# Optimization experiments

Hardware: AMD Instinct MI355X
Metric: run time of the kernel (lower is better)

## Reference

```python
import jax, jax.numpy as jnp
import numpy as np

NUM_HEADS = 12
DROP_RATIO = 0.25
LN_EPS = 1e-5


def _layernorm(x, g, b):
    m = jnp.mean(x, axis=-1, keepdims=True)
    v = jnp.var(x, axis=-1, keepdims=True)
    return (x - m) * jax.lax.rsqrt(v + LN_EPS) * g + b


def setup_inputs() -> dict:
    key = jax.random.key(0)
    ks = jax.random.split(key, 12)
    B, N, C = 16, 785, 768
    H = 4 * C
    s = 0.02
    return {
        "x": jax.random.normal(ks[0], (B, N, C), dtype=jnp.float32),
        "ln1_g": jnp.ones((C,), jnp.float32),
        "ln1_b": jnp.zeros((C,), jnp.float32),
        "w_qkv": jax.random.normal(ks[1], (C, 3 * C), jnp.float32) * s,  # qkv_bias=False
        "w_proj": jax.random.normal(ks[2], (C, C), jnp.float32) * s,
        "b_proj": jnp.zeros((C,), jnp.float32),
        "ln2_g": jnp.ones((C,), jnp.float32),
        "ln2_b": jnp.zeros((C,), jnp.float32),
        "w_fc1": jax.random.normal(ks[3], (C, H), jnp.float32) * s,
        "b_fc1": jnp.zeros((H,), jnp.float32),
        "w_fc2": jax.random.normal(ks[4], (H, C), jnp.float32) * s,
        "b_fc2": jnp.zeros((C,), jnp.float32),
    }


def _block(x, ln1_g, ln1_b, w_qkv, w_proj, b_proj, ln2_g, ln2_b,
           w_fc1, b_fc1, w_fc2, b_fc2):
    B, N, C = x.shape
    Hh = NUM_HEADS
    Dh = C // Hh
    scale = Dh ** -0.5
    target = N - int(N * DROP_RATIO)  # kept KV length (incl. CLS)

    h = _layernorm(x, ln1_g, ln1_b)
    qkv = (h @ w_qkv).reshape(B, N, 3, Hh, Dh).transpose(2, 0, 3, 1, 4)
    q, k, v = qkv[0], qkv[1], qkv[2]  # each [B, H, N, Dh]

    # 'low' branch: L2-norm token scoring on non-CLS k tokens, keep top (target-1)
    rem_k = k[:, :, 1:, :]
    rem_v = v[:, :, 1:, :]
    scores = jnp.linalg.norm(rem_k, axis=-1) / Dh  # [B, H, N-1]
    _, idx = jax.lax.top_k(scores, target - 1)
    idx = jnp.sort(idx, axis=-1)  # restore original token order
    idx_e = idx[..., None]
    new_k = jnp.concatenate(
        [k[:, :, :1, :], jnp.take_along_axis(rem_k, idx_e, axis=2)], axis=2)
    new_v = jnp.concatenate(
        [v[:, :, :1, :], jnp.take_along_axis(rem_v, idx_e, axis=2)], axis=2)

    attn = jnp.einsum('bhnd,bhmd->bhnm', q, new_k) * scale
    attn = jax.nn.softmax(attn, axis=-1)
    o = jnp.einsum('bhnm,bhmd->bhnd', attn, new_v)
    o = o.transpose(0, 2, 1, 3).reshape(B, N, C)
    o = o @ w_proj + b_proj
    x = x + o  # drop_path = 0

    h2 = _layernorm(x, ln2_g, ln2_b)
    m = jax.nn.gelu(h2 @ w_fc1 + b_fc1, approximate=False) @ w_fc2 + b_fc2
    return x + m


def reference(x, ln1_g, ln1_b, w_qkv, w_proj, b_proj, ln2_g, ln2_b,
              w_fc1, b_fc1, w_fc2, b_fc2):
    return _block(x, ln1_g, ln1_b, w_qkv, w_proj, b_proj, ln2_g, ln2_b,
                  w_fc1, b_fc1, w_fc2, b_fc2)
```

## Files before the change

kernel.cpp:

```cpp
#include <hip/hip_runtime.h>

#define B_ 16
#define NTOK 785
#define C_ 768
#define HH 12
#define DH 64
#define BHN (B_*HH)
#define KVLEN 589
#define KVPAD 640
#define MROWS (B_*785)
#define HID 3072

typedef __bf16  bf16x8  __attribute__((ext_vector_type(8)));
typedef short   short4v __attribute__((ext_vector_type(4)));
typedef float   f32x4   __attribute__((ext_vector_type(4)));
typedef int     int4v   __attribute__((ext_vector_type(4)));
typedef unsigned short u16;
typedef signed char i8;

__device__ __forceinline__ u16 f2b(float f) {
  unsigned u = __builtin_bit_cast(unsigned, f);
  u = u + 0x7FFFu + ((u >> 16) & 1u);
  return (u16)(u >> 16);
}

#define SH_I8   (127.0f / 6.0f)
#define SW1_I8  (127.0f / 0.125f)
#define DEQ1    ((6.0f * 0.125f) / (127.0f * 127.0f))
#define SG_I8   (127.0f / 4.0f)
#define SW2_I8  (127.0f / 0.12f)
#define DEQ2    ((4.0f * 0.12f) / (127.0f * 127.0f))

#define QSCALE  0.18033688011112042f

__device__ __forceinline__ i8 f2i8(float v, float s) {
  float q = rintf(v * s);
  q = fminf(127.0f, fmaxf(-127.0f, q));
  return (i8)(int)q;
}

__device__ __forceinline__ float gelu_f(float x) {
  float ax = fabsf(x) * 0.70710678118654752f;
  float t  = __builtin_amdgcn_rcpf(1.0f + 0.3275911f * ax);
  float y  = t * (0.254829592f + t * (-0.284496736f + t * (1.421413741f +
             t * (-1.453152027f + t * 1.061405429f))));
  float er = 1.0f - y * __expf(-ax * ax);
  er = copysignf(er, x);
  return 0.5f * x * (1.0f + er);
}

#define AS1C(p) ((const __attribute__((address_space(1))) void*)(p))
#define AS3(p)  ((__attribute__((address_space(3))) void*)(p))
#define SWZ(row, g) ((row)*64 + ((((g) ^ ((row)&7))) << 3))
#define SWZ8B(row, g) ((row)*128 + ((((g) ^ ((row)&7))) << 4))

#define OFF_H   ((size_t)0)
#define OFF_KF  ((size_t)19292160)
#define OFF_QB  (OFF_KF + (size_t)38584320)
#define OFF_VB  (OFF_QB + (size_t)19292160)
#define OFF_KP  (OFF_VB + (size_t)19292160)
#define OFF_VP  (OFF_KP + (size_t)15728640)
#define OFF_OB  (OFF_VP + (size_t)15728640)
#define OFF_WQ  (OFF_OB + (size_t)19292160)
#define OFF_WP  (OFF_WQ + (size_t)3538944)
#define OFF_W1  (OFF_WP + (size_t)1179648)
#define OFF_W2  (OFF_W1 + (size_t)4718592)
#define OFF_SC  (OFF_W2 + (size_t)4718592)
#define OFF_IX  (OFF_SC + (size_t)602112)
#define OFF_G   OFF_KF

__global__ __launch_bounds__(256)
void transpose_cast(const float* __restrict__ w, u16* __restrict__ wt, int K, int N) {
  __shared__ float T[64][65];
  const int k0 = blockIdx.x * 64, n0 = blockIdx.y * 64;
  const int tid = threadIdx.x;
  const int cc = tid & 63, rr = tid >> 6;
#pragma unroll
  for (int i = 0; i < 16; ++i) {
    int r = rr + i * 4;
    T[r][cc] = w[(size_t)(k0 + r) * N + n0 + cc];
  }
  __syncthreads();
#pragma unroll
  for (int i = 0; i < 16; ++i) {
    int r = rr + i * 4;
    wt[(size_t)(n0 + r) * K + k0 + cc] = f2b(T[cc][r]);
  }
}

__global__ __launch_bounds__(256)
void transpose_quant(const float* __restrict__ w, i8* __restrict__ wt, int K, int N,
                     float scale) {
  __shared__ float T[64][65];
  const int k0 = blockIdx.x * 64, n0 = blockIdx.y * 64;
  const int tid = threadIdx.x;
  const int cc = tid & 63, rr = tid >> 6;
#pragma unroll
  for (int i = 0; i < 16; ++i) {
    int r = rr + i * 4;
    T[r][cc] = w[(size_t)(k0 + r) * N + n0 + cc];
  }
  __syncthreads();
#pragma unroll
  for (int i = 0; i < 16; ++i) {
    int r = rr + i * 4;
    wt[(size_t)(n0 + r) * K + k0 + cc] = f2i8(T[cc][r], scale);
  }
}

__global__ __launch_bounds__(256)
void ln_kernel(const float* __restrict__ x, const float* __restrict__ g,
               const float* __restrict__ b, u16* __restrict__ out) {
  const int row = blockIdx.x;
  const int tid = threadIdx.x;
  const float* xr = x + (size_t)row * C_;
  float v0 = xr[tid], v1 = xr[tid + 256], v2 = xr[tid + 512];
  float sum = v0 + v1 + v2;
  float sq  = v0 * v0 + v1 * v1 + v2 * v2;
#pragma unroll
  for (int o = 32; o > 0; o >>= 1) { sum += __shfl_xor(sum, o); sq += __shfl_xor(sq, o); }
  __shared__ float rs[4], rq[4];
  int w = tid >> 6;
  if ((tid & 63) == 0) { rs[w] = sum; rq[w] = sq; }
  __syncthreads();
  sum = rs[0] + rs[1] + rs[2] + rs[3];
  sq  = rq[0] + rq[1] + rq[2] + rq[3];
  float mean = sum * (1.0f / C_);
  float var  = sq * (1.0f / C_) - mean * mean;
  float rstd = rsqrtf(var + 1e-5f);
  u16* orow = out + (size_t)row * C_;
  orow[tid]       = f2b((v0 - mean) * rstd * g[tid]       + b[tid]);
  orow[tid + 256] = f2b((v1 - mean) * rstd * g[tid + 256] + b[tid + 256]);
  orow[tid + 512] = f2b((v2 - mean) * rstd * g[tid + 512] + b[tid + 512]);
}

__global__ __launch_bounds__(256)
void ln_kernel_i8(const float* __restrict__ x, const float* __restrict__ g,
                  const float* __restrict__ b, i8* __restrict__ out) {
  const int row = blockIdx.x;
  const int tid = threadIdx.x;
  const float* xr = x + (size_t)row * C_;
  float v0 = xr[tid], v1 = xr[tid + 256], v2 = xr[tid + 512];
  float sum = v0 + v1 + v2;
  float sq  = v0 * v0 + v1 * v1 + v2 * v2;
#pragma unroll
  for (int o = 32; o > 0; o >>= 1) { sum += __shfl_xor(sum, o); sq += __shfl_xor(sq, o); }
  __shared__ float rs[4], rq[4];
  int w = tid >> 6;
  if ((tid & 63) == 0) { rs[w] = sum; rq[w] = sq; }
  __syncthreads();
  sum = rs[0] + rs[1] + rs[2] + rs[3];
  sq  = rq[0] + rq[1] + rq[2] + rq[3];
  float mean = sum * (1.0f / C_);
  float var  = sq * (1.0f / C_) - mean * mean;
  float rstd = rsqrtf(var + 1e-5f);
  i8* orow = out + (size_t)row * C_;
  orow[tid]       = f2i8((v0 - mean) * rstd * g[tid]       + b[tid],       SH_I8);
  orow[tid + 256] = f2i8((v1 - mean) * rstd * g[tid + 256] + b[tid + 256], SH_I8);
  orow[tid + 512] = f2i8((v2 - mean) * rstd * g[tid + 512] + b[tid + 512], SH_I8);
}

template<int EPI>
__global__ __launch_bounds__(256, 2)
void gemm128(const u16* __restrict__ A, const u16* __restrict__ Bt,
             int M, int N, int K,
             const float* __restrict__ bias, const float* __restrict__ addsrc,
             float* __restrict__ outf, u16* __restrict__ outb,
             u16* __restrict__ qb, u16* __restrict__ kb, u16* __restrict__ vb,
             float* __restrict__ sc) {
  __shared__ u16 As[128 * 64];
  __shared__ u16 Bs[128 * 64];
  const int tid = threadIdx.x;
  const int lane = tid & 63;
  const int w = tid >> 6;
  const int wm = w >> 1, wn = w & 1;
  const int l15 = lane & 15;
  const int hi = lane >> 4;

  const int CN = (N + 127) >> 7;
  const int nwg = gridDim.x * gridDim.y;
  const int orig = blockIdx.x + blockIdx.y * gridDim.x;
  const int q = nwg >> 3, r8 = nwg & 7;
  const int xcd = orig & 7, pos = orig >> 3;
  const int wgid = (xcd < r8 ? xcd * (q + 1) : r8 * (q + 1) + (xcd - r8) * q) + pos;
  const int m0 = (wgid / CN) * 128;
  const int n0 = (wgid - (wgid / CN) * CN) * 128;

  const int srow = tid >> 3;
  const int sseg = tid & 7;

  f32x4 acc[4][4] = {};

  for (int kt = 0; kt < K; kt += 64) {
    __syncthreads();
#pragma unroll
    for (int i = 0; i < 4; ++i) {
      int row = i * 32 + srow;
      int gseg = sseg ^ (row & 7);
      int gr = m0 + row; if (gr >= M) gr = M - 1;
      int flat = i * 256 + tid;
      __builtin_amdgcn_global_load_lds(AS1C(A  + (size_t)gr * K         + kt + gseg * 8),
                                       AS3(&As[flat * 8]), 16, 0, 0);
      __builtin_amdgcn_global_load_lds(AS1C(Bt + (size_t)(n0 + row) * K + kt + gseg * 8),
                                       AS3(&Bs[flat * 8]), 16, 0, 0);
    }
    __syncthreads();
#pragma unroll
    for (int kk = 0; kk < 2; ++kk) {
      bf16x8 a[4], b[4];
#pragma unroll
      for (int mi = 0; mi < 4; ++mi)
        a[mi] = *reinterpret_cast<const bf16x8*>(&As[SWZ(wm * 64 + mi * 16 + l15, kk * 4 + hi)]);
#pragma unroll
      for (int ni = 0; ni < 4; ++ni)
        b[ni] = *reinterpret_cast<const bf16x8*>(&Bs[SWZ(wn * 64 + ni * 16 + l15, kk * 4 + hi)]);
#pragma unroll
      for (int mi = 0; mi < 4; ++mi)
#pragma unroll
        for (int ni = 0; ni < 4; ++ni)
          acc[mi][ni] = __builtin_amdgcn_mfma_f32_16x16x32_bf16(a[mi], b[ni], acc[mi][ni], 0, 0, 0);
    }
  }

#pragma unroll
  for (int mi = 0; mi < 4; ++mi) {
#pragma unroll
    for (int ni = 0; ni < 4; ++ni) {
#pragma unroll
      for (int j = 0; j < 4; ++j) {
        int r = m0 + wm * 64 + mi * 16 + hi * 4 + j;
        int c = n0 + wn * 64 + ni * 16 + l15;
        if (r < M) {
          float v = acc[mi][ni][j];
          if (EPI == 0) {
            int sec = (c >= 1536) ? 2 : (c >= 768 ? 1 : 0);
            int cm = c - sec * 768;
            int hh = cm >> 6, d = cm & 63;
            int bb = r / NTOK; int nn = r - bb * NTOK;
            size_t addr = (((size_t)(bb * HH + hh)) * NTOK + nn) * DH + d;
            if (sec == 0)      qb[addr] = f2b(v * QSCALE);
            else if (sec == 1) kb[addr] = f2b(v);
            else               vb[addr] = f2b(v);
          } else {
            size_t o = (size_t)r * N + c;
            outf[o] = v + bias[c] + addsrc[o];
          }
        }
      }
    }
  }

  if (EPI == 0) {
    int csec = n0 + wn * 64;
    if (csec >= 768 && csec < 1536) {
      int hh = (csec - 768) >> 6;
#pragma unroll
      for (int mi = 0; mi < 4; ++mi) {
#pragma unroll
        for (int j = 0; j < 4; ++j) {
          float ss = 0.0f;
#pragma unroll
          for (int ni = 0; ni < 4; ++ni) { float v = acc[mi][ni][j]; ss += v * v; }
          ss += __shfl_xor(ss, 1); ss += __shfl_xor(ss, 2);
          ss += __shfl_xor(ss, 4); ss += __shfl_xor(ss, 8);
          int r = m0 + wm * 64 + mi * 16 + hi * 4 + j;
          if (l15 == 0 && r < M) {
            int bb = r / NTOK, nn = r - bb * NTOK;
            if (nn >= 1)
              sc[(size_t)(bb * HH + hh) * 784 + nn - 1] = sqrtf(ss) * (1.0f / 64.0f);
          }
        }
      }
    }
  }
}

template<int EPI>
__global__ __launch_bounds__(256, 2)
void gemm128_i8(const i8* __restrict__ A, const i8* __restrict__ Bt,
                int M, int N, int K, float deq,
                const float* __restrict__ bias, const float* __restrict__ addsrc,
                float* __restrict__ outf, i8* __restrict__ outq) {
  __shared__ i8 As[128 * 128];
  __shared__ i8 Bs[128 * 128];
  const int tid = threadIdx.x;
  const int lane = tid & 63;
  const int w = tid >> 6;
  const int wm = w >> 1, wn = w & 1;
  const int l15 = lane & 15;
  const int hi = lane >> 4;

  const int CN = (N + 127) >> 7;
  const int nwg = gridDim.x * gridDim.y;
  const int orig = blockIdx.x + blockIdx.y * gridDim.x;
  const int q = nwg >> 3, r8 = nwg & 7;
  const int xcd = orig & 7, pos = orig >> 3;
  const int wgid = (xcd < r8 ? xcd * (q + 1) : r8 * (q + 1) + (xcd - r8) * q) + pos;
  const int m0 = (wgid / CN) * 128;
  const int n0 = (wgid - (wgid / CN) * CN) * 128;

  const int srow = tid >> 3;
  const int sg   = tid & 7;

  int4v acc[4][4] = {};

  for (int kt = 0; kt < K; kt += 128) {
    __syncthreads();
#pragma unroll
    for (int i = 0; i < 4; ++i) {
      int row = i * 32 + srow;
      int gsw = sg ^ (row & 7);
      int gr = m0 + row; if (gr >= M) gr = M - 1;
      int flat = i * 256 + tid;
      __builtin_amdgcn_global_load_lds(AS1C(A  + (size_t)gr * K         + kt + gsw * 16),
                                       AS3(&As[flat * 16]), 16, 0, 0);
      __builtin_amdgcn_global_load_lds(AS1C(Bt + (size_t)(n0 + row) * K + kt + gsw * 16),
                                       AS3(&Bs[flat * 16]), 16, 0, 0);
    }
    __syncthreads();
#pragma unroll
    for (int kk = 0; kk < 2; ++kk) {
      int4v a[4], b[4];
#pragma unroll
      for (int mi = 0; mi < 4; ++mi) {
        int R = wm * 64 + mi * 16 + l15;
        a[mi] = *reinterpret_cast<const int4v*>(&As[SWZ8B(R, kk * 4 + hi)]);
      }
#pragma unroll
      for (int ni = 0; ni < 4; ++ni) {
        int R = wn * 64 + ni * 16 + l15;
        b[ni] = *reinterpret_cast<const int4v*>(&Bs[SWZ8B(R, kk * 4 + hi)]);
      }
#pragma unroll
      for (int mi = 0; mi < 4; ++mi)
#pragma unroll
        for (int ni = 0; ni < 4; ++ni)
          acc[mi][ni] = __builtin_amdgcn_mfma_i32_16x16x64_i8(a[mi], b[ni], acc[mi][ni], 0, 0, 0);
    }
  }

#pragma unroll
  for (int mi = 0; mi < 4; ++mi) {
#pragma unroll
    for (int ni = 0; ni < 4; ++ni) {
#pragma unroll
      for (int j = 0; j < 4; ++j) {
        int r = m0 + wm * 64 + mi * 16 + hi * 4 + j;
        int c = n0 + wn * 64 + ni * 16 + l15;
        if (r < M) {
          float t = (float)acc[mi][ni][j] * deq + bias[c];
          if (EPI == 2) {
            outq[(size_t)r * N + c] = f2i8(gelu_f(t), SG_I8);
          } else {
            size_t o = (size_t)r * N + c;
            outf[o] = t + addsrc[o];
          }
        }
      }
    }
  }
}

__global__ __launch_bounds__(512)
void topk_kernel(const float* __restrict__ scores, int* __restrict__ idxb) {
  const int bh = blockIdx.x;
  const int tid = threadIdx.x;
  __shared__ float ss[1024];
  __shared__ int   sid[1024];
  __shared__ int   sid2[1024];
  for (int i = tid; i < 1024; i += 512) {
    ss[i]  = (i < 784) ? scores[bh * 784 + i] : -__builtin_inff();
    sid[i] = i;
  }
  for (int k = 2; k <= 1024; k <<= 1) {
    for (int j = k >> 1; j > 0; j >>= 1) {
      __syncthreads();
      for (int i = tid; i < 1024; i += 512) {
        int ixj = i ^ j;
        if (ixj > i) {
          float s1 = ss[i], s2 = ss[ixj];
          int   i1 = sid[i], i2 = sid[ixj];
          bool keep = (s1 > s2) || (s1 == s2 && i1 < i2);
          bool doSwap = ((i & k) == 0) ? !keep : keep;
          if (doSwap) { ss[i] = s2; ss[ixj] = s1; sid[i] = i2; sid[ixj] = i1; }
        }
      }
    }
  }
  __syncthreads();
  for (int i = tid; i < 1024; i += 512)
    sid2[i] = (i < 588) ? sid[i] : 0x7FFFFFFF;
  for (int k = 2; k <= 1024; k <<= 1) {
    for (int j = k >> 1; j > 0; j >>= 1) {
      __syncthreads();
      for (int i = tid; i < 1024; i += 512) {
        int ixj = i ^ j;
        if (ixj > i) {
          int a = sid2[i], b2 = sid2[ixj];
          bool keep = (a < b2);
          bool doSwap = ((i & k) == 0) ? !keep : keep;
          if (doSwap) { sid2[i] = b2; sid2[ixj] = a; }
        }
      }
    }
  }
  __syncthreads();
  for (int i = tid; i < 588; i += 512) idxb[bh * 588 + i] = sid2[i];
}

__global__ __launch_bounds__(256)
void gather_kernel(const u16* __restrict__ kb, const u16* __restrict__ vb,
                   const int* __restrict__ idxb, u16* __restrict__ kp, u16* __restrict__ vpT) {
  __shared__ u16 T[64 * 64];
  const int bh = blockIdx.x, chunk = blockIdx.y, t = threadIdx.x;
  {
    int jl = t >> 2, d0 = (t & 3) * 16;
    int j = chunk * 64 + jl;
    int n = (j == 0) ? 0 : (j <= 588 ? idxb[bh * 588 + j - 1] + 1 : -1);
    int4v k0 = {}, k1 = {}, v0 = {}, v1 = {};
    if (n >= 0) {
      size_t src = ((size_t)bh * NTOK + n) * DH + d0;
      k0 = *reinterpret_cast<const int4v*>(&kb[src]);
      k1 = *reinterpret_cast<const int4v*>(&kb[src + 8]);
      v0 = *reinterpret_cast<const int4v*>(&vb[src]);
      v1 = *reinterpret_cast<const int4v*>(&vb[src + 8]);
    }
    size_t kdst = ((size_t)bh * KVPAD + j) * DH + d0;
    *reinterpret_cast<int4v*>(&kp[kdst])     = k0;
    *reinterpret_cast<int4v*>(&kp[kdst + 8]) = k1;
    *reinterpret_cast<int4v*>(&T[jl * 64 + d0])     = v0;
    *reinterpret_cast<int4v*>(&T[jl * 64 + d0 + 8]) = v1;
  }
  __syncthreads();
  {
    int d = t & 63, kvo = (t >> 6) * 16;
    const int swp = ((d >> 3) & 1) * 4;
    alignas(16) u16 tmp[16];
#pragma unroll
    for (int i = 0; i < 16; ++i) tmp[i ^ swp] = T[(kvo + i) * 64 + d];
    size_t dst = ((size_t)bh * 64 + d) * KVPAD + chunk * 64 + kvo;
    *reinterpret_cast<int4v*>(&vpT[dst])     = *reinterpret_cast<int4v*>(&tmp[0]);
    *reinterpret_cast<int4v*>(&vpT[dst + 8]) = *reinterpret_cast<int4v*>(&tmp[8]);
  }
}

__global__ __launch_bounds__(256)
void attn_kernel(const u16* __restrict__ qb, const u16* __restrict__ kp,
                 const u16* __restrict__ vpT, u16* __restrict__ ob) {
  __shared__ u16 Qs[64 * 64];
  __shared__ u16 Ks[64 * 64];
  __shared__ u16 VTs[64 * 64];
  const int tid = threadIdx.x;
  const int lane = tid & 63;
  const int w = tid >> 6;
  const int l15 = lane & 15;
  const int hi = lane >> 4;
  const int hswp = (l15 >> 3) & 1;

  const int nwg = gridDim.x;
  const int orig = blockIdx.x;
  const int q = nwg >> 3, r8 = nwg & 7;
  const int xcd = orig & 7, pos = orig >> 3;
  const int wgid = (xcd < r8 ? xcd * (q + 1) : r8 * (q + 1) + (xcd - r8) * q) + pos;
  const int bh = wgid / 13;
  const int n0 = (wgid - bh * 13) * 64;

#pragma unroll
  for (int i = 0; i < 2; ++i) {
    int flat = i * 256 + tid;
    int row = flat >> 3, g = flat & 7;
    int4v val = {};
    if (n0 + row < NTOK)
      val = *reinterpret_cast<const int4v*>(qb + ((size_t)bh * NTOK + n0 + row) * DH + g * 8);
    *reinterpret_cast<int4v*>(&Qs[SWZ(row, g)]) = val;
  }
  __syncthreads();
  bf16x8 q0 = *reinterpret_cast<const bf16x8*>(&Qs[SWZ(w * 16 + l15, hi)]);
  bf16x8 q1 = *reinterpret_cast<const bf16x8*>(&Qs[SWZ(w * 16 + l15, 4 + hi)]);

  float m_run = -__builtin_inff(), l_run = 0.0f;
  f32x4 oa[4] = {};

#define ATTN_STEP(KVT, MASKED)                                                    \
  {                                                                               \
    int4v kr[2], vr[2];                                                           \
    _Pragma("unroll")                                                             \
    for (int i = 0; i < 2; ++i) {                                                 \
      int flat = i * 256 + tid;                                                   \
      int row = flat >> 3, g = flat & 7;                                          \
      kr[i] = *reinterpret_cast<const int4v*>(                                    \
          kp  + ((size_t)bh * KVPAD + (KVT) * 64 + row) * DH + g * 8);            \
      vr[i] = *reinterpret_cast<const int4v*>(                                    \
          vpT + ((size_t)bh * 64 + row) * KVPAD + (KVT) * 64 + g * 8);            \
    }                                                                             \
    __syncthreads();                                                              \
    _Pragma("unroll")                                                             \
    for (int i = 0; i < 2; ++i) {                                                 \
      int flat = i * 256 + tid;                                                   \
      int row = flat >> 3, g = flat & 7;                                          \
      *reinterpret_cast<int4v*>(&Ks[SWZ(row, g)])  = kr[i];                       \
      *reinterpret_cast<int4v*>(&VTs[SWZ(row, g)]) = vr[i];                       \
    }                                                                             \
    __syncthreads();                                                              \
    f32x4 st[4];                                                                  \
    _Pragma("unroll")                                                             \
    for (int ft = 0; ft < 4; ++ft) {                                              \
      bf16x8 a0 = *reinterpret_cast<const bf16x8*>(&Ks[SWZ(ft * 16 + l15, hi)]);  \
      bf16x8 a1 = *reinterpret_cast<const bf16x8*>(&Ks[SWZ(ft * 16 + l15, 4 + hi)]); \
      f32x4 cfr = {};                                                             \
      cfr = __builtin_amdgcn_mfma_f32_16x16x32_bf16(a0, q0, cfr, 0, 0, 0);        \
      cfr = __builtin_amdgcn_mfma_f32_16x16x32_bf16(a1, q1, cfr, 0, 0, 0);        \
      if (MASKED) {                                                               \
        _Pragma("unroll")                                                         \
        for (int j = 0; j < 4; ++j) {                                             \
          int kv = (KVT) * 64 + ft * 16 + hi * 4 + j;                             \
          if (kv >= KVLEN) cfr[j] = -3.0e38f;                                     \
        }                                                                         \
      }                                                                           \
      st[ft] = cfr;                                                               \
    }                                                                             \
    float mx = fmaxf(fmaxf(st[0][0], st[0][1]), fmaxf(st[0][2], st[0][3]));       \
    _Pragma("unroll")                                                             \
    for (int ft = 1; ft < 4; ++ft)                                                \
      mx = fmaxf(mx, fmaxf(fmaxf(st[ft][0], st[ft][1]), fmaxf(st[ft][2], st[ft][3]))); \
    mx = fmaxf(mx, __shfl_xor(mx, 16));                                           \
    mx = fmaxf(mx, __shfl_xor(mx, 32));                                           \
    float m_new = fmaxf(m_run, mx);                                               \
    float alpha = exp2f(m_run - m_new);                                           \
    float psum = 0.0f;                                                            \
    short4v pb[4];                                                                \
    _Pragma("unroll")                                                             \
    for (int ft = 0; ft < 4; ++ft) {                                              \
      _Pragma("unroll")                                                           \
      for (int j = 0; j < 4; ++j) {                                               \
        float p = exp2f(st[ft][j] - m_new);                                       \
        psum += p;                                                                \
        pb[ft][j] = (short)(u16)(__builtin_bit_cast(unsigned, p) >> 16);          \
      }                                                                           \
    }                                                                             \
    psum += __shfl_xor(psum, 16);                                                 \
    psum += __shfl_xor(psum, 32);                                                 \
    l_run = l_run * alpha + psum;                                                 \
    m_run = m_new;                                                                \
    _Pragma("unroll")                                                             \
    for (int df = 0; df < 4; ++df) {                                              \
      oa[df][0] *= alpha; oa[df][1] *= alpha; oa[df][2] *= alpha; oa[df][3] *= alpha; \
    }                                                                             \
    _Pragma("unroll")                                                             \
    for (int df = 0; df < 4; ++df) {                                              \
      _Pragma("unroll")                                                           \
      for (int ft = 0; ft < 4; ++ft) {                                            \
        short4v va = *reinterpret_cast<const short4v*>(                           \
            &VTs[SWZ(df * 16 + l15, ft * 2 + (hi >> 1)) + (((hi & 1) ^ hswp)) * 4]); \
        oa[df] = __builtin_amdgcn_mfma_f32_16x16x16bf16_1k(va, pb[ft], oa[df], 0, 0, 0); \
      }                                                                           \
    }                                                                             \
  }

  for (int kvt = 0; kvt < 9; ++kvt) {
    ATTN_STEP(kvt, false)
  }
  ATTN_STEP(9, true)
#undef ATTN_STEP

  int n = n0 + w * 16 + l15;
  if (n < NTOK) {
    float inv = 1.0f / l_run;
    int bb = bh / HH, hh = bh - bb * HH;
    size_t base = ((size_t)bb * NTOK + n) * C_ + hh * DH;
#pragma unroll
    for (int df = 0; df < 4; ++df) {
      short4v pv;
#pragma unroll
      for (int j = 0; j < 4; ++j) pv[j] = (short)f2b(oa[df][j] * inv);
      *reinterpret_cast<short4v*>(ob + base + df * 16 + hi * 4) = pv;
    }
  }
}

extern "C" void kernel_launch(void* const* d_in, const int* in_sizes, int n_in,
                              void* d_out, int out_size, void* d_ws, size_t ws_size,
                              hipStream_t stream) {
  const float* x     = (const float*)d_in[0];
  const float* ln1g  = (const float*)d_in[1];
  const float* ln1b  = (const float*)d_in[2];
  const float* wqkv  = (const float*)d_in[3];
  const float* wproj = (const float*)d_in[4];
  const float* bproj = (const float*)d_in[5];
  const float* ln2g  = (const float*)d_in[6];
  const float* ln2b  = (const float*)d_in[7];
  const float* wfc1  = (const float*)d_in[8];
  const float* bfc1  = (const float*)d_in[9];
  const float* wfc2  = (const float*)d_in[10];
  const float* bfc2  = (const float*)d_in[11];
  float* out = (float*)d_out;
  char* wsb = (char*)d_ws;

  u16*   h     = (u16*)(wsb + OFF_H);
  i8*    hq    = (i8*)(wsb + OFF_H);
  u16*   kb    = (u16*)(wsb + OFF_KF);
  u16*   qb    = (u16*)(wsb + OFF_QB);
  u16*   vb    = (u16*)(wsb + OFF_VB);
  u16*   kp    = (u16*)(wsb + OFF_KP);
  u16*   vpT   = (u16*)(wsb + OFF_VP);
  u16*   ob    = (u16*)(wsb + OFF_OB);
  u16*   wqT   = (u16*)(wsb + OFF_WQ);
  u16*   wpT   = (u16*)(wsb + OFF_WP);
  i8*    w1q   = (i8*)(wsb + OFF_W1);
  i8*    w2q   = (i8*)(wsb + OFF_W2);
  float* sc    = (float*)(wsb + OFF_SC);
  int*   idxb  = (int*)(wsb + OFF_IX);
  i8*    gq    = (i8*)(wsb + OFF_G);

  transpose_cast<<<dim3(768 / 64, 2304 / 64), 256, 0, stream>>>(wqkv, wqT, 768, 2304);
  transpose_cast<<<dim3(768 / 64, 768 / 64),  256, 0, stream>>>(wproj, wpT, 768, 768);
  transpose_quant<<<dim3(768 / 64, 3072 / 64), 256, 0, stream>>>(wfc1, w1q, 768, 3072, SW1_I8);
  transpose_quant<<<dim3(3072 / 64, 768 / 64), 256, 0, stream>>>(wfc2, w2q, 3072, 768, SW2_I8);

  ln_kernel<<<MROWS, 256, 0, stream>>>(x, ln1g, ln1b, h);

  gemm128<0><<<dim3(2304 / 128, 99), 256, 0, stream>>>(h, wqT, MROWS, 2304, 768,
      nullptr, nullptr, nullptr, nullptr, qb, kb, vb, sc);

  topk_kernel<<<BHN, 512, 0, stream>>>(sc, idxb);
  gather_kernel<<<dim3(BHN, KVPAD / 64), 256, 0, stream>>>(kb, vb, idxb, kp, vpT);

  attn_kernel<<<BHN * 13, 256, 0, stream>>>(qb, kp, vpT, ob);

  gemm128<1><<<dim3(768 / 128, 99), 256, 0, stream>>>(ob, wpT, MROWS, 768, 768,
      bproj, x, out, nullptr, nullptr, nullptr, nullptr, nullptr);

  ln_kernel_i8<<<MROWS, 256, 0, stream>>>(out, ln2g, ln2b, hq);

  gemm128_i8<2><<<dim3(3072 / 128, 99), 256, 0, stream>>>(hq, w1q, MROWS, 3072, 768,
      DEQ1, bfc1, nullptr, nullptr, gq);

  gemm128_i8<3><<<dim3(768 / 128, 99), 256, 0, stream>>>(gq, w2q, MROWS, 768, 3072,
      DEQ2, bfc2, out, out, nullptr);
}
```

Measured before the change: 391.3 us.

## Process 128 query rows per attention workgroup to reuse K/V tiles

Each attention workgroup now handles 128 query rows instead of 64, with every wave computing two 16-row query blocks against the same K and V tiles held in shared memory. This halves the number of K/V tile loads from global memory and the barriers per query row, and gives each wave more independent MFMA work to interleave. In exchange it raises register pressure, since two sets of accumulators and softmax state are live, and cuts the grid from 13 to 7 chunks per head, which wastes more padded rows in the last chunk and lowers workgroup count.

```diff
diff --git a/kernel.cpp b/kernel.cpp
--- a/kernel.cpp
+++ b/kernel.cpp
@@ -10,6 +10,7 @@
 #define KVPAD 640
 #define MROWS (B_*785)
 #define HID 3072
+#define QCH 7
 
 typedef __bf16  bf16x8  __attribute__((ext_vector_type(8)));
 typedef short   short4v __attribute__((ext_vector_type(4)));
@@ -447,7 +448,7 @@
 __global__ __launch_bounds__(256)
 void attn_kernel(const u16* __restrict__ qb, const u16* __restrict__ kp,
                  const u16* __restrict__ vpT, u16* __restrict__ ob) {
-  __shared__ u16 Qs[64 * 64];
+  __shared__ u16 Qs[128 * 64];
   __shared__ u16 Ks[64 * 64];
   __shared__ u16 VTs[64 * 64];
   const int tid = threadIdx.x;
@@ -462,11 +463,11 @@
   const int q = nwg >> 3, r8 = nwg & 7;
   const int xcd = orig & 7, pos = orig >> 3;
   const int wgid = (xcd < r8 ? xcd * (q + 1) : r8 * (q + 1) + (xcd - r8) * q) + pos;
-  const int bh = wgid / 13;
-  const int n0 = (wgid - bh * 13) * 64;
-
-#pragma unroll
-  for (int i = 0; i < 2; ++i) {
+  const int bh = wgid / QCH;
+  const int n0 = (wgid - bh * QCH) * 128;
+
+#pragma unroll
+  for (int i = 0; i < 4; ++i) {
     int flat = i * 256 + tid;
     int row = flat >> 3, g = flat & 7;
     int4v val = {};
@@ -475,11 +476,15 @@
     *reinterpret_cast<int4v*>(&Qs[SWZ(row, g)]) = val;
   }
   __syncthreads();
-  bf16x8 q0 = *reinterpret_cast<const bf16x8*>(&Qs[SWZ(w * 16 + l15, hi)]);
-  bf16x8 q1 = *reinterpret_cast<const bf16x8*>(&Qs[SWZ(w * 16 + l15, 4 + hi)]);
-
-  float m_run = -__builtin_inff(), l_run = 0.0f;
-  f32x4 oa[4] = {};
+  const int rA = w * 32 + l15, rB = rA + 16;
+  bf16x8 qa0 = *reinterpret_cast<const bf16x8*>(&Qs[SWZ(rA, hi)]);
+  bf16x8 qa1 = *reinterpret_cast<const bf16x8*>(&Qs[SWZ(rA, 4 + hi)]);
+  bf16x8 qb0 = *reinterpret_cast<const bf16x8*>(&Qs[SWZ(rB, hi)]);
+  bf16x8 qb1 = *reinterpret_cast<const bf16x8*>(&Qs[SWZ(rB, 4 + hi)]);
+
+  float mA = -__builtin_inff(), lA = 0.0f;
+  float mB = -__builtin_inff(), lB = 0.0f;
+  f32x4 oaA[4] = {}, oaB[4] = {};
 
 #define ATTN_STEP(KVT, MASKED)                                                    \
   {                                                                               \
@@ -502,49 +507,57 @@
       *reinterpret_cast<int4v*>(&VTs[SWZ(row, g)]) = vr[i];                       \
     }                                                                             \
     __syncthreads();                                                              \
-    f32x4 st[4];                                                                  \
+    f32x4 stA[4], stB[4];                                                         \
     _Pragma("unroll")                                                             \
     for (int ft = 0; ft < 4; ++ft) {                                              \
       bf16x8 a0 = *reinterpret_cast<const bf16x8*>(&Ks[SWZ(ft * 16 + l15, hi)]);  \
       bf16x8 a1 = *reinterpret_cast<const bf16x8*>(&Ks[SWZ(ft * 16 + l15, 4 + hi)]); \
-      f32x4 cfr = {};                                                             \
-      cfr = __builtin_amdgcn_mfma_f32_16x16x32_bf16(a0, q0, cfr, 0, 0, 0);        \
-      cfr = __builtin_amdgcn_mfma_f32_16x16x32_bf16(a1, q1, cfr, 0, 0, 0);        \
+      f32x4 cA = {}, cB = {};                                                     \
+      cA = __builtin_amdgcn_mfma_f32_16x16x32_bf16(a0, qa0, cA, 0, 0, 0);         \
+      cA = __builtin_amdgcn_mfma_f32_16x16x32_bf16(a1, qa1, cA, 0, 0, 0);         \
+      cB = __builtin_amdgcn_mfma_f32_16x16x32_bf16(a0, qb0, cB, 0, 0, 0);         \
+      cB = __builtin_amdgcn_mfma_f32_16x16x32_bf16(a1, qb1, cB, 0, 0, 0);         \
       if (MASKED) {                                                               \
         _Pragma("unroll")                                                         \
         for (int j = 0; j < 4; ++j) {                                             \
           int kv = (KVT) * 64 + ft * 16 + hi * 4 + j;                             \
-          if (kv >= KVLEN) cfr[j] = -3.0e38f;                                     \
+          if (kv >= KVLEN) { cA[j] = -3.0e38f; cB[j] = -3.0e38f; }                \
         }                                                                         \
       }                                                                           \
-      st[ft] = cfr;                                                               \
+      stA[ft] = cA; stB[ft] = cB;                                                 \
     }                                                                             \
-    float mx = fmaxf(fmaxf(st[0][0], st[0][1]), fmaxf(st[0][2], st[0][3]));       \
+    float mxA = fmaxf(fmaxf(stA[0][0], stA[0][1]), fmaxf(stA[0][2], stA[0][3]));  \
+    float mxB = fmaxf(fmaxf(stB[0][0], stB[0][1]), fmaxf(stB[0][2], stB[0][3]));  \
     _Pragma("unroll")                                                             \
-    for (int ft = 1; ft < 4; ++ft)                                                \
-      mx = fmaxf(mx, fmaxf(fmaxf(st[ft][0], st[ft][1]), fmaxf(st[ft][2], st[ft][3]))); \
-    mx = fmaxf(mx, __shfl_xor(mx, 16));                                           \
-    mx = fmaxf(mx, __shfl_xor(mx, 32));                                           \
-    float m_new = fmaxf(m_run, mx);                                               \
-    float alpha = exp2f(m_run - m_new);                                           \
-    float psum = 0.0f;                                                            \
-    short4v pb[4];                                                                \
+    for (int ft = 1; ft < 4; ++ft) {                                              \
+      mxA = fmaxf(mxA, fmaxf(fmaxf(stA[ft][0], stA[ft][1]), fmaxf(stA[ft][2], stA[ft][3]))); \
+      mxB = fmaxf(mxB, fmaxf(fmaxf(stB[ft][0], stB[ft][1]), fmaxf(stB[ft][2], stB[ft][3]))); \
+    }                                                                             \
+    mxA = fmaxf(mxA, __shfl_xor(mxA, 16)); mxA = fmaxf(mxA, __shfl_xor(mxA, 32)); \
+    mxB = fmaxf(mxB, __shfl_xor(mxB, 16)); mxB = fmaxf(mxB, __shfl_xor(mxB, 32)); \
+    float mnA = fmaxf(mA, mxA), mnB = fmaxf(mB, mxB);                             \
+    float alA = exp2f(mA - mnA), alB = exp2f(mB - mnB);                           \
+    float psA = 0.0f, psB = 0.0f;                                                 \
+    short4v pbA[4], pbB[4];                                                       \
     _Pragma("unroll")                                                             \
     for (int ft = 0; ft < 4; ++ft) {                                              \
       _Pragma("unroll")                                                           \
       for (int j = 0; j < 4; ++j) {                                               \
-        float p = exp2f(st[ft][j] - m_new);                                       \
-        psum += p;                                                                \
-        pb[ft][j] = (short)(u16)(__builtin_bit_cast(unsigned, p) >> 16);          \
+        float pA = exp2f(stA[ft][j] - mnA);                                       \
+        float pB = exp2f(stB[ft][j] - mnB);                                       \
+        psA += pA; psB += pB;                                                     \
+        pbA[ft][j] = (short)(u16)(__builtin_bit_cast(unsigned, pA) >> 16);        \
+        pbB[ft][j] = (short)(u16)(__builtin_bit_cast(unsigned, pB) >> 16);        \
       }                                                                           \
     }                                                                             \
-    psum += __shfl_xor(psum, 16);                                                 \
-    psum += __shfl_xor(psum, 32);                                                 \
-    l_run = l_run * alpha + psum;                                                 \
-    m_run = m_new;                                                                \
+    psA += __shfl_xor(psA, 16); psA += __shfl_xor(psA, 32);                       \
+    psB += __shfl_xor(psB, 16); psB += __shfl_xor(psB, 32);                       \
+    lA = lA * alA + psA; mA = mnA;                                                \
+    lB = lB * alB + psB; mB = mnB;                                                \
     _Pragma("unroll")                                                             \
     for (int df = 0; df < 4; ++df) {                                              \
-      oa[df][0] *= alpha; oa[df][1] *= alpha; oa[df][2] *= alpha; oa[df][3] *= alpha; \
+      oaA[df][0] *= alA; oaA[df][1] *= alA; oaA[df][2] *= alA; oaA[df][3] *= alA; \
+      oaB[df][0] *= alB; oaB[df][1] *= alB; oaB[df][2] *= alB; oaB[df][3] *= alB; \
     }                                                                             \
     _Pragma("unroll")                                                             \
     for (int df = 0; df < 4; ++df) {                                              \
@@ -552,7 +565,8 @@
       for (int ft = 0; ft < 4; ++ft) {                                            \
         short4v va = *reinterpret_cast<const short4v*>(                           \
             &VTs[SWZ(df * 16 + l15, ft * 2 + (hi >> 1)) + (((hi & 1) ^ hswp)) * 4]); \
-        oa[df] = __builtin_amdgcn_mfma_f32_16x16x16bf16_1k(va, pb[ft], oa[df], 0, 0, 0); \
+        oaA[df] = __builtin_amdgcn_mfma_f32_16x16x16bf16_1k(va, pbA[ft], oaA[df], 0, 0, 0); \
+        oaB[df] = __builtin_amdgcn_mfma_f32_16x16x16bf16_1k(va, pbB[ft], oaB[df], 0, 0, 0); \
       }                                                                           \
     }                                                                             \
   }
@@ -563,17 +577,33 @@
   ATTN_STEP(9, true)
 #undef ATTN_STEP
 
-  int n = n0 + w * 16 + l15;
-  if (n < NTOK) {
-    float inv = 1.0f / l_run;
-    int bb = bh / HH, hh = bh - bb * HH;
-    size_t base = ((size_t)bb * NTOK + n) * C_ + hh * DH;
-#pragma unroll
-    for (int df = 0; df < 4; ++df) {
-      short4v pv;
-#pragma unroll
-      for (int j = 0; j < 4; ++j) pv[j] = (short)f2b(oa[df][j] * inv);
-      *reinterpret_cast<short4v*>(ob + base + df * 16 + hi * 4) = pv;
+  const int bb = bh / HH, hh = bh - bb * HH;
+  {
+    int n = n0 + rA;
+    if (n < NTOK) {
+      float inv = 1.0f / lA;
+      size_t base = ((size_t)bb * NTOK + n) * C_ + hh * DH;
+#pragma unroll
+      for (int df = 0; df < 4; ++df) {
+        short4v pv;
+#pragma unroll
+        for (int j = 0; j < 4; ++j) pv[j] = (short)f2b(oaA[df][j] * inv);
+        *reinterpret_cast<short4v*>(ob + base + df * 16 + hi * 4) = pv;
+      }
+    }
+  }
+  {
+    int n = n0 + rB;
+    if (n < NTOK) {
+      float inv = 1.0f / lB;
+      size_t base = ((size_t)bb * NTOK + n) * C_ + hh * DH;
+#pragma unroll
+      for (int df = 0; df < 4; ++df) {
+        short4v pv;
+#pragma unroll
+        for (int j = 0; j < 4; ++j) pv[j] = (short)f2b(oaB[df][j] * inv);
+        *reinterpret_cast<short4v*>(ob + base + df * 16 + hi * 4) = pv;
+      }
     }
   }
 }
@@ -625,7 +655,7 @@
   topk_kernel<<<BHN, 512, 0, stream>>>(sc, idxb);
   gather_kernel<<<dim3(BHN, KVPAD / 64), 256, 0, stream>>>(kb, vb, idxb, kp, vpT);
 
-  attn_kernel<<<BHN * 13, 256, 0, stream>>>(qb, kp, vpT, ob);
+  attn_kernel<<<BHN * QCH, 256, 0, stream>>>(qb, kp, vpT, ob);
 
   gemm128<1><<<dim3(768 / 128, 99), 256, 0, stream>>>(ob, wpT, MROWS, 768, 768,
       bproj, x, out, nullptr, nullptr, nullptr, nullptr, nullptr);
```

New measurement: 408.6 us. 1.04x slower.

## Split QKV GEMM: keep K in bf16, compute Q and V with int8 MFMA

Applied to the files above, without the earlier changes.

The fused bf16 QKV projection is split in two. K, which drives the top-k token scoring, stays in bf16. Q and V now come from an int8 GEMM that reads an int8 copy of the first LayerNorm output, written by a new dual-output LN kernel. The goal is higher MFMA throughput for two thirds of the QKV work. In exchange it adds an extra launch, more LN writes, and quantization error in Q and V, with fixed weight scales reused from FC1.

```diff
diff --git a/kernel.cpp b/kernel.cpp
--- a/kernel.cpp
+++ b/kernel.cpp
@@ -70,7 +70,8 @@
 #define OFF_G   OFF_KF
 
 __global__ __launch_bounds__(256)
-void transpose_cast(const float* __restrict__ w, u16* __restrict__ wt, int K, int N) {
+void transpose_cast(const float* __restrict__ w, u16* __restrict__ wt, int K, int N,
+                    int strideN) {
   __shared__ float T[64][65];
   const int k0 = blockIdx.x * 64, n0 = blockIdx.y * 64;
   const int tid = threadIdx.x;
@@ -78,7 +79,7 @@
 #pragma unroll
   for (int i = 0; i < 16; ++i) {
     int r = rr + i * 4;
-    T[r][cc] = w[(size_t)(k0 + r) * N + n0 + cc];
+    T[r][cc] = w[(size_t)(k0 + r) * strideN + n0 + cc];
   }
   __syncthreads();
 #pragma unroll
@@ -90,7 +91,7 @@
 
 __global__ __launch_bounds__(256)
 void transpose_quant(const float* __restrict__ w, i8* __restrict__ wt, int K, int N,
-                     float scale) {
+                     int strideN, float scale) {
   __shared__ float T[64][65];
   const int k0 = blockIdx.x * 64, n0 = blockIdx.y * 64;
   const int tid = threadIdx.x;
@@ -98,7 +99,7 @@
 #pragma unroll
   for (int i = 0; i < 16; ++i) {
     int r = rr + i * 4;
-    T[r][cc] = w[(size_t)(k0 + r) * N + n0 + cc];
+    T[r][cc] = w[(size_t)(k0 + r) * strideN + n0 + cc];
   }
   __syncthreads();
 #pragma unroll
@@ -109,8 +110,9 @@
 }
 
 __global__ __launch_bounds__(256)
-void ln_kernel(const float* __restrict__ x, const float* __restrict__ g,
-               const float* __restrict__ b, u16* __restrict__ out) {
+void ln_kernel_dual(const float* __restrict__ x, const float* __restrict__ g,
+                    const float* __restrict__ b, u16* __restrict__ out,
+                    i8* __restrict__ outq) {
   const int row = blockIdx.x;
   const int tid = threadIdx.x;
   const float* xr = x + (size_t)row * C_;
@@ -129,9 +131,13 @@
   float var  = sq * (1.0f / C_) - mean * mean;
   float rstd = rsqrtf(var + 1e-5f);
   u16* orow = out + (size_t)row * C_;
-  orow[tid]       = f2b((v0 - mean) * rstd * g[tid]       + b[tid]);
-  orow[tid + 256] = f2b((v1 - mean) * rstd * g[tid + 256] + b[tid + 256]);
-  orow[tid + 512] = f2b((v2 - mean) * rstd * g[tid + 512] + b[tid + 512]);
+  i8*  qrow = outq + (size_t)row * C_;
+  float h0 = (v0 - mean) * rstd * g[tid]       + b[tid];
+  float h1 = (v1 - mean) * rstd * g[tid + 256] + b[tid + 256];
+  float h2 = (v2 - mean) * rstd * g[tid + 512] + b[tid + 512];
+  orow[tid]       = f2b(h0); qrow[tid]       = f2i8(h0, SH_I8);
+  orow[tid + 256] = f2b(h1); qrow[tid + 256] = f2i8(h1, SH_I8);
+  orow[tid + 512] = f2b(h2); qrow[tid + 512] = f2i8(h2, SH_I8);
 }
 
 __global__ __launch_bounds__(256)
@@ -165,8 +171,7 @@
 void gemm128(const u16* __restrict__ A, const u16* __restrict__ Bt,
              int M, int N, int K,
              const float* __restrict__ bias, const float* __restrict__ addsrc,
-             float* __restrict__ outf, u16* __restrict__ outb,
-             u16* __restrict__ qb, u16* __restrict__ kb, u16* __restrict__ vb,
+             float* __restrict__ outf, u16* __restrict__ kb,
              float* __restrict__ sc) {
   __shared__ u16 As[128 * 64];
   __shared__ u16 Bs[128 * 64];
@@ -232,15 +237,10 @@
         int c = n0 + wn * 64 + ni * 16 + l15;
         if (r < M) {
           float v = acc[mi][ni][j];
-          if (EPI == 0) {
-            int sec = (c >= 1536) ? 2 : (c >= 768 ? 1 : 0);
-            int cm = c - sec * 768;
-            int hh = cm >> 6, d = cm & 63;
+          if (EPI == 4) {
+            int hh = c >> 6, d = c & 63;
             int bb = r / NTOK; int nn = r - bb * NTOK;
-            size_t addr = (((size_t)(bb * HH + hh)) * NTOK + nn) * DH + d;
-            if (sec == 0)      qb[addr] = f2b(v * QSCALE);
-            else if (sec == 1) kb[addr] = f2b(v);
-            else               vb[addr] = f2b(v);
+            kb[(((size_t)(bb * HH + hh)) * NTOK + nn) * DH + d] = f2b(v);
           } else {
             size_t o = (size_t)r * N + c;
             outf[o] = v + bias[c] + addsrc[o];
@@ -250,25 +250,22 @@
     }
   }
 
-  if (EPI == 0) {
-    int csec = n0 + wn * 64;
-    if (csec >= 768 && csec < 1536) {
-      int hh = (csec - 768) >> 6;
-#pragma unroll
-      for (int mi = 0; mi < 4; ++mi) {
-#pragma unroll
-        for (int j = 0; j < 4; ++j) {
-          float ss = 0.0f;
-#pragma unroll
-          for (int ni = 0; ni < 4; ++ni) { float v = acc[mi][ni][j]; ss += v * v; }
-          ss += __shfl_xor(ss, 1); ss += __shfl_xor(ss, 2);
-          ss += __shfl_xor(ss, 4); ss += __shfl_xor(ss, 8);
-          int r = m0 + wm * 64 + mi * 16 + hi * 4 + j;
-          if (l15 == 0 && r < M) {
-            int bb = r / NTOK, nn = r - bb * NTOK;
-            if (nn >= 1)
-              sc[(size_t)(bb * HH + hh) * 784 + nn - 1] = sqrtf(ss) * (1.0f / 64.0f);
-          }
+  if (EPI == 4) {
+    int hh = (n0 + wn * 64) >> 6;
+#pragma unroll
+    for (int mi = 0; mi < 4; ++mi) {
+#pragma unroll
+      for (int j = 0; j < 4; ++j) {
+        float ss = 0.0f;
+#pragma unroll
+        for (int ni = 0; ni < 4; ++ni) { float v = acc[mi][ni][j]; ss += v * v; }
+        ss += __shfl_xor(ss, 1); ss += __shfl_xor(ss, 2);
+        ss += __shfl_xor(ss, 4); ss += __shfl_xor(ss, 8);
+        int r = m0 + wm * 64 + mi * 16 + hi * 4 + j;
+        if (l15 == 0 && r < M) {
+          int bb = r / NTOK, nn = r - bb * NTOK;
+          if (nn >= 1)
+            sc[(size_t)(bb * HH + hh) * 784 + nn - 1] = sqrtf(ss) * (1.0f / 64.0f);
         }
       }
     }
@@ -280,7 +277,8 @@
 void gemm128_i8(const i8* __restrict__ A, const i8* __restrict__ Bt,
                 int M, int N, int K, float deq,
                 const float* __restrict__ bias, const float* __restrict__ addsrc,
-                float* __restrict__ outf, i8* __restrict__ outq) {
+                float* __restrict__ outf, i8* __restrict__ outq,
+                u16* __restrict__ qb, u16* __restrict__ vb) {
   __shared__ i8 As[128 * 128];
   __shared__ i8 Bs[128 * 128];
   const int tid = threadIdx.x;
@@ -348,12 +346,22 @@
         int r = m0 + wm * 64 + mi * 16 + hi * 4 + j;
         int c = n0 + wn * 64 + ni * 16 + l15;
         if (r < M) {
-          float t = (float)acc[mi][ni][j] * deq + bias[c];
+          float t = (float)acc[mi][ni][j] * deq;
           if (EPI == 2) {
+            t += bias[c];
             outq[(size_t)r * N + c] = f2i8(gelu_f(t), SG_I8);
-          } else {
+          } else if (EPI == 3) {
+            t += bias[c];
             size_t o = (size_t)r * N + c;
             outf[o] = t + addsrc[o];
+          } else {
+            int isV = (c >= 768);
+            int cm = c - (isV ? 768 : 0);
+            int hh = cm >> 6, d = cm & 63;
+            int bb = r / NTOK; int nn = r - bb * NTOK;
+            size_t addr = (((size_t)(bb * HH + hh)) * NTOK + nn) * DH + d;
+            if (isV) vb[addr] = f2b(t);
+            else     qb[addr] = f2b(t * QSCALE);
           }
         }
       }
@@ -604,7 +612,9 @@
   u16*   kp    = (u16*)(wsb + OFF_KP);
   u16*   vpT   = (u16*)(wsb + OFF_VP);
   u16*   ob    = (u16*)(wsb + OFF_OB);
-  u16*   wqT   = (u16*)(wsb + OFF_WQ);
+  i8*    hq1   = (i8*)(wsb + OFF_OB);
+  u16*   wkT   = (u16*)(wsb + OFF_WQ);
+  i8*    wqvq  = (i8*)(wsb + OFF_WQ + 1179648);
   u16*   wpT   = (u16*)(wsb + OFF_WP);
   i8*    w1q   = (i8*)(wsb + OFF_W1);
   i8*    w2q   = (i8*)(wsb + OFF_W2);
@@ -612,15 +622,20 @@
   int*   idxb  = (int*)(wsb + OFF_IX);
   i8*    gq    = (i8*)(wsb + OFF_G);
 
-  transpose_cast<<<dim3(768 / 64, 2304 / 64), 256, 0, stream>>>(wqkv, wqT, 768, 2304);
-  transpose_cast<<<dim3(768 / 64, 768 / 64),  256, 0, stream>>>(wproj, wpT, 768, 768);
-  transpose_quant<<<dim3(768 / 64, 3072 / 64), 256, 0, stream>>>(wfc1, w1q, 768, 3072, SW1_I8);
-  transpose_quant<<<dim3(3072 / 64, 768 / 64), 256, 0, stream>>>(wfc2, w2q, 3072, 768, SW2_I8);
-
-  ln_kernel<<<MROWS, 256, 0, stream>>>(x, ln1g, ln1b, h);
-
-  gemm128<0><<<dim3(2304 / 128, 99), 256, 0, stream>>>(h, wqT, MROWS, 2304, 768,
-      nullptr, nullptr, nullptr, nullptr, qb, kb, vb, sc);
+  transpose_cast <<<dim3(768 / 64, 768 / 64),  256, 0, stream>>>(wqkv + 768,  wkT, 768, 768, 2304);
+  transpose_quant<<<dim3(768 / 64, 768 / 64),  256, 0, stream>>>(wqkv,        wqvq, 768, 768, 2304, SW1_I8);
+  transpose_quant<<<dim3(768 / 64, 768 / 64),  256, 0, stream>>>(wqkv + 1536, wqvq + 768 * 768, 768, 768, 2304, SW1_I8);
+  transpose_cast <<<dim3(768 / 64, 768 / 64),  256, 0, stream>>>(wproj, wpT, 768, 768, 768);
+  transpose_quant<<<dim3(768 / 64, 3072 / 64), 256, 0, stream>>>(wfc1, w1q, 768, 3072, 3072, SW1_I8);
+  transpose_quant<<<dim3(3072 / 64, 768 / 64), 256, 0, stream>>>(wfc2, w2q, 3072, 768, 768, SW2_I8);
+
+  ln_kernel_dual<<<MROWS, 256, 0, stream>>>(x, ln1g, ln1b, h, hq1);
+
+  gemm128<4><<<dim3(768 / 128, 99), 256, 0, stream>>>(h, wkT, MROWS, 768, 768,
+      nullptr, nullptr, nullptr, kb, sc);
+
+  gemm128_i8<4><<<dim3(1536 / 128, 99), 256, 0, stream>>>(hq1, wqvq, MROWS, 1536, 768,
+      DEQ1, nullptr, nullptr, nullptr, nullptr, qb, vb);
 
   topk_kernel<<<BHN, 512, 0, stream>>>(sc, idxb);
   gather_kernel<<<dim3(BHN, KVPAD / 64), 256, 0, stream>>>(kb, vb, idxb, kp, vpT);
@@ -628,13 +643,13 @@
   attn_kernel<<<BHN * 13, 256, 0, stream>>>(qb, kp, vpT, ob);
 
   gemm128<1><<<dim3(768 / 128, 99), 256, 0, stream>>>(ob, wpT, MROWS, 768, 768,
-      bproj, x, out, nullptr, nullptr, nullptr, nullptr, nullptr);
+      bproj, x, out, nullptr, nullptr);
 
   ln_kernel_i8<<<MROWS, 256, 0, stream>>>(out, ln2g, ln2b, hq);
 
   gemm128_i8<2><<<dim3(3072 / 128, 99), 256, 0, stream>>>(hq, w1q, MROWS, 3072, 768,
-      DEQ1, bfc1, nullptr, nullptr, gq);
+      DEQ1, bfc1, nullptr, nullptr, gq, nullptr, nullptr);
 
   gemm128_i8<3><<<dim3(768 / 128, 99), 256, 0, stream>>>(gq, w2q, MROWS, 768, 3072,
-      DEQ2, bfc2, out, out, nullptr);
-}
+      DEQ2, bfc2, out, out, nullptr, nullptr, nullptr);
+}
```

Measured after the change: 391.6 us. About the same (+0.1%).
